# Kernel optimization log

Hardware: AMD Instinct MI355X
Metric: run time of the kernel (lower is better)

Reference implementation:

```python
import jax, jax.numpy as jnp
import numpy as np

ALPHA = 0.5
EPS = 1e-10

def setup_inputs() -> dict:
    key = jax.random.key(0)
    k1, k2, k3, k4 = jax.random.split(key, 4)
    B, S, H = 8, 2048, 768
    query_embs = jax.random.normal(k1, (B, S, H), dtype=jnp.float32)
    key_embs = jax.random.normal(k2, (B, S, H), dtype=jnp.float32)
    q_mask = (jax.random.uniform(k3, (B, S)) > 0.1).astype(jnp.float32)
    k_mask = (jax.random.uniform(k4, (B, S)) > 0.1).astype(jnp.float32)
    q_mask = q_mask.at[:, 0].set(1.0)
    k_mask = k_mask.at[:, 0].set(1.0)
    return {"query_embs": query_embs, "key_embs": key_embs,
            "q_mask": q_mask, "k_mask": k_mask, "gumbel_temp": 1.0}

def _l2norm(x):
    # torch F.normalize: x / max(||x||, eps-ish); use rsqrt with tiny floor
    n = jnp.sqrt(jnp.sum(x * x, axis=-1, keepdims=True))
    return x / jnp.maximum(n, 1e-12)

def reference(query_embs, key_embs, q_mask, k_mask, gumbel_temp):
    B, S, H = query_embs.shape
    q = _l2norm(query_embs)
    k = _l2norm(key_embs)
    sim = jnp.einsum('bqh,bkh->bqk', q, k)  # [B,S,S]
    # exponential distance decay w_{ij} = exp(-alpha*|i-j|)
    pos = jnp.arange(S)
    dist = jnp.abs(pos[:, None] - pos[None, :]).astype(sim.dtype)
    sim = sim * jnp.exp(-ALPHA * dist)
    valid = q_mask[:, :, None] * k_mask[:, None, :]  # [B,S,S]
    # eval path: no Gumbel noise
    noisy = sim / gumbel_temp
    noisy = noisy * valid - (1.0 - valid) * 1e9
    p = jax.nn.softmax(noisy, axis=-1)
    agg = jnp.einsum('bqk,bkh->bqh', p, k)
    scores = jnp.sum(q * agg, axis=-1) * q_mask  # [B,S]
    denom = jnp.maximum(jnp.sum(q_mask, axis=-1), 1.0)
    return jnp.sum(scores, axis=-1) / denom  # [B]
```

## Files before the change

kernel.cpp:

```cpp
#include <hip/hip_runtime.h>
#include <math.h>

#define SB 8
#define SS 2048
#define SH 768
#define ALPHA 0.5f

typedef __fp16 f16x8 __attribute__((ext_vector_type(8)));
typedef float f32x4 __attribute__((ext_vector_type(4)));

__device__ __forceinline__ float dot4(float4 a, float4 b) {
  return a.x*b.x + a.y*b.y + a.z*b.z + a.w*b.w;
}
__device__ __forceinline__ unsigned int pk2(float a, float b) {
  return __builtin_bit_cast(unsigned int, __builtin_amdgcn_cvt_pkrtz(a, b));
}

#define GLD(d, p, imm) \
  asm volatile("global_load_dwordx4 %0, %1, off offset:" #imm \
               : "=v"(d) : "v"(p) : "memory")
#define WAITV(n) asm volatile("s_waitcnt vmcnt(" #n ")" ::: "memory")
#define SB0() __builtin_amdgcn_sched_barrier(0)

#define ISSUE6(P, R0, R1, R2, R3, R4, R5) do { \
  GLD(R0, P, 0);   GLD(R1, P, 64);  GLD(R2, P, 128); \
  GLD(R3, P, 192); GLD(R4, P, 256); GLD(R5, P, 320); } while (0)

#define MFMA(a, b, c) __builtin_amdgcn_mfma_f32_16x16x32_f16(a, b, c, 0, 0, 0)

#define FTILE(t, R0, R1, R2, R3, R4, R5) do { \
  f32x4 da_ = {0,0,0,0}, db_ = {0,0,0,0}; \
  da_ = MFMA(a0, R0, da_); db_ = MFMA(a1, R1, db_); \
  da_ = MFMA(a2, R2, da_); db_ = MFMA(a3, R3, db_); \
  da_ = MFMA(a4, R4, da_); db_ = MFMA(a5, R5, db_); \
  sP[w][t][lane] = da_ + db_; } while (0)


__global__ __launch_bounds__(256) void kprep_kernel(
    const float* __restrict__ K, const float* __restrict__ km,
    const float* __restrict__ qm,
    __fp16* __restrict__ Khs, float* __restrict__ ksum,
    float* __restrict__ Nk, float* __restrict__ qsum) {
  __shared__ float4 red[4][3][64];
  int b = blockIdx.y, jc = blockIdx.x, t = threadIdx.x;
  int w = t >> 6, lane = t & 63;
  int j0 = jc * 32;
  float4 acc0 = {0,0,0,0}, acc1 = {0,0,0,0}, acc2 = {0,0,0,0};
  for (int jj = 0; jj < 8; ++jj) {
    int j = j0 + 8 * w + jj;
    const float4* rp = (const float4*)(K + ((size_t)b * SS + j) * SH);
    float4 a = rp[lane], b4 = rp[lane + 64], c4 = rp[lane + 128];
    float ssv = dot4(a, a) + dot4(b4, b4) + dot4(c4, c4);
    #pragma unroll
    for (int m = 1; m < 64; m <<= 1) ssv += __shfl_xor(ssv, m, 64);
    float kwj = km[b * SS + j] / fmaxf(sqrtf(ssv), 1e-12f);
    uint2* kr = (uint2*)(Khs + ((size_t)b * SS + j) * SH);
    kr[lane]       = make_uint2(pk2(a.x*kwj,  a.y*kwj),  pk2(a.z*kwj,  a.w*kwj));
    kr[lane + 64]  = make_uint2(pk2(b4.x*kwj, b4.y*kwj), pk2(b4.z*kwj, b4.w*kwj));
    kr[lane + 128] = make_uint2(pk2(c4.x*kwj, c4.y*kwj), pk2(c4.z*kwj, c4.w*kwj));
    acc0.x += a.x*kwj;  acc0.y += a.y*kwj;  acc0.z += a.z*kwj;  acc0.w += a.w*kwj;
    acc1.x += b4.x*kwj; acc1.y += b4.y*kwj; acc1.z += b4.z*kwj; acc1.w += b4.w*kwj;
    acc2.x += c4.x*kwj; acc2.y += c4.y*kwj; acc2.z += c4.z*kwj; acc2.w += c4.w*kwj;
  }
  red[w][0][lane] = acc0; red[w][1][lane] = acc1; red[w][2][lane] = acc2;
  __syncthreads();
  if (t < 192) {
    int s = t >> 6, l = t & 63;
    float4 r0 = red[0][s][l], r1 = red[1][s][l], r2 = red[2][s][l], r3 = red[3][s][l];
    float* kp = ksum + b * SH + (s * 64 + l) * 4;
    atomicAdd(kp + 0, r0.x+r1.x+r2.x+r3.x);
    atomicAdd(kp + 1, r0.y+r1.y+r2.y+r3.y);
    atomicAdd(kp + 2, r0.z+r1.z+r2.z+r3.z);
    atomicAdd(kp + 3, r0.w+r1.w+r2.w+r3.w);
  }
  if (t < 32) {
    float pkm = km[b * SS + j0 + t];
    float pqm = qm[b * SS + j0 + t];
    #pragma unroll
    for (int m = 1; m < 32; m <<= 1) {
      pkm += __shfl_xor(pkm, m, 64);
      pqm += __shfl_xor(pqm, m, 64);
    }
    if (t == 0) { atomicAdd(&Nk[b], pkm); atomicAdd(&qsum[b], pqm); }
  }
}

__global__ __launch_bounds__(256)
__attribute__((amdgpu_waves_per_eu(4, 4)))
void band_kernel(
    const float* __restrict__ Q, const __fp16* __restrict__ Khs,
    const float* __restrict__ temp, const float* __restrict__ qm,
    const float* __restrict__ ksum, const float* __restrict__ Nkp,
    const float* __restrict__ qsum,
    float* __restrict__ acc, int* __restrict__ cnt, float* __restrict__ out) {
  __shared__ f32x4 sP[4][5][64];
  __shared__ float sSS[4][16], sDD[4][16];
  __shared__ float tab_s[64];
  int tid = threadIdx.x;
  int w = tid >> 6, lane = tid & 63;
  int l15 = lane & 15, quad = lane >> 4;
  int blk = blockIdx.x;
  int work = (blk & 7) * 128 + (blk >> 3);
  int b = work >> 7;
  int i0 = (work & 127) * 16;

  if (tid < 64) {
    float invt = 1.0f / temp[0];
    tab_s[tid] = __expf(-ALPHA * fabsf((float)(tid - 31))) * invt;
  }
  float nk = Nkp[b];

  const char* qpB = (const char*)(Q + ((size_t)b * SS + i0 + l15) * SH
                                  + w * 192 + quad * 8);
  const float* ksb = ksum + (size_t)b * SH + w * 192 + quad * 8;
  float4 x0, x1, x2, x3, x4, x5, x6, x7, x8, x9, x10, x11;
  GLD(x0, qpB, 0);    GLD(x1, qpB, 16);   GLD(x2, qpB, 128);
  GLD(x3, qpB, 144);  GLD(x4, qpB, 256);  GLD(x5, qpB, 272);
  GLD(x6, qpB, 384);  GLD(x7, qpB, 400);  GLD(x8, qpB, 512);
  GLD(x9, qpB, 528);  GLD(x10, qpB, 640); GLD(x11, qpB, 656);
  float4 g0  = *(const float4*)(ksb + 0);
  float4 g1  = *(const float4*)(ksb + 4);
  float4 g2  = *(const float4*)(ksb + 32);
  float4 g3  = *(const float4*)(ksb + 36);
  float4 g4  = *(const float4*)(ksb + 64);
  float4 g5  = *(const float4*)(ksb + 68);
  float4 g6  = *(const float4*)(ksb + 96);
  float4 g7  = *(const float4*)(ksb + 100);
  float4 g8  = *(const float4*)(ksb + 128);
  float4 g9  = *(const float4*)(ksb + 132);
  float4 g10 = *(const float4*)(ksb + 160);
  float4 g11 = *(const float4*)(ksb + 164);
  WAITV(0); SB0();

  float ss = dot4(x0,x0) + dot4(x1,x1) + dot4(x2,x2) + dot4(x3,x3)
           + dot4(x4,x4) + dot4(x5,x5) + dot4(x6,x6) + dot4(x7,x7)
           + dot4(x8,x8) + dot4(x9,x9) + dot4(x10,x10) + dot4(x11,x11);
  float dd = dot4(x0,g0) + dot4(x1,g1) + dot4(x2,g2) + dot4(x3,g3)
           + dot4(x4,g4) + dot4(x5,g5) + dot4(x6,g6) + dot4(x7,g7)
           + dot4(x8,g8) + dot4(x9,g9) + dot4(x10,g10) + dot4(x11,g11);
  #define MKA(a, xA, xB) do { \
    uint4 u_ = make_uint4(pk2(xA.x, xA.y), pk2(xA.z, xA.w), \
                          pk2(xB.x, xB.y), pk2(xB.z, xB.w)); \
    a = __builtin_bit_cast(f16x8, u_); } while (0)
  f16x8 a0, a1, a2, a3, a4, a5;
  MKA(a0, x0, x1); MKA(a1, x2, x3); MKA(a2, x4, x5);
  MKA(a3, x6, x7); MKA(a4, x8, x9); MKA(a5, x10, x11);

  ss += __shfl_xor(ss, 16, 64); ss += __shfl_xor(ss, 32, 64);
  dd += __shfl_xor(dd, 16, 64); dd += __shfl_xor(dd, 32, 64);
  if (quad == 0) { sSS[w][l15] = ss; sDD[w][l15] = dd; }

  const __fp16* KbH = Khs + (size_t)b * SS * SH;
  int jc0 = min(max(i0 - 32 + l15, 0), SS - 1);
  int jc1 = min(max(i0 - 16 + l15, 0), SS - 1);
  int jc2 = i0 + l15;
  int jc3 = min(i0 + 16 + l15, SS - 1);
  int jc4 = min(i0 + 32 + l15, SS - 1);
  const char* pt0 = (const char*)(KbH + (size_t)jc0 * SH + w * 192 + quad * 8);
  const char* pt1 = (const char*)(KbH + (size_t)jc1 * SH + w * 192 + quad * 8);
  const char* pt2 = (const char*)(KbH + (size_t)jc2 * SH + w * 192 + quad * 8);
  const char* pt3 = (const char*)(KbH + (size_t)jc3 * SH + w * 192 + quad * 8);
  const char* pt4 = (const char*)(KbH + (size_t)jc4 * SH + w * 192 + quad * 8);

  f16x8 B0, B1, B2, B3, B4, B5, C0, C1, C2, C3, C4, C5;
  ISSUE6(pt0, B0, B1, B2, B3, B4, B5);
  ISSUE6(pt1, C0, C1, C2, C3, C4, C5);
  WAITV(6); SB0(); FTILE(0, B0, B1, B2, B3, B4, B5);
  ISSUE6(pt2, B0, B1, B2, B3, B4, B5);
  WAITV(6); SB0(); FTILE(1, C0, C1, C2, C3, C4, C5);
  ISSUE6(pt3, C0, C1, C2, C3, C4, C5);
  WAITV(6); SB0(); FTILE(2, B0, B1, B2, B3, B4, B5);
  ISSUE6(pt4, B0, B1, B2, B3, B4, B5);
  WAITV(6); SB0(); FTILE(3, C0, C1, C2, C3, C4, C5);
  WAITV(0); SB0(); FTILE(4, B0, B1, B2, B3, B4, B5);

  __syncthreads();

  float qws[4], d0s[4];
  #pragma unroll
  for (int reg = 0; reg < 4; ++reg) {
    int r = quad * 4 + reg;
    float ssr = sSS[0][r] + sSS[1][r] + sSS[2][r] + sSS[3][r];
    float ddr = sDD[0][r] + sDD[1][r] + sDD[2][r] + sDD[3][r];
    qws[reg] = qm[b * SS + i0 + r] / fmaxf(sqrtf(ssr), 1e-12f);
    d0s[reg] = ddr;
  }
  float an[4] = {0,0,0,0}, ad[4] = {0,0,0,0};
  #pragma unroll
  for (int t = 0; t < 5; ++t) {
    f32x4 v = sP[0][t][lane] + sP[1][t][lane] + sP[2][t][lane] + sP[3][t][lane];
    int j = i0 - 32 + 16 * t + l15;
    float vmask = ((unsigned)j < SS) ? 1.0f : 0.0f;
    int idxb = 16 * t + l15 - 1;
    #pragma unroll
    for (int reg = 0; reg < 4; ++reg) {
      float sv = v[reg] * qws[reg];
      int idx = min(max(idxb - quad * 4 - reg, 0), 63);
      float ev = (__expf(sv * tab_s[idx]) - 1.0f) * vmask;
      an[reg] += ev * sv;
      ad[reg] += ev;
    }
  }
  float tot = 0.f;
  #pragma unroll
  for (int reg = 0; reg < 4; ++reg) {
    float a = an[reg], e = ad[reg];
    a += __shfl_xor(a, 1, 64); a += __shfl_xor(a, 2, 64);
    a += __shfl_xor(a, 4, 64); a += __shfl_xor(a, 8, 64);
    e += __shfl_xor(e, 1, 64); e += __shfl_xor(e, 2, 64);
    e += __shfl_xor(e, 4, 64); e += __shfl_xor(e, 8, 64);
    tot += (qws[reg] * d0s[reg] + a) / (nk + e);
  }
  tot += __shfl_xor(tot, 16, 64);
  tot += __shfl_xor(tot, 32, 64);
  if (tid == 0) {
    atomicAdd(&acc[b], tot);
    __threadfence();
    if (atomicAdd(&cnt[b], 1) == 127) {
      float a2 = atomicAdd(&acc[b], 0.0f);
      out[b] = a2 / fmaxf(qsum[b], 1.0f);
    }
  }
}

extern "C" void kernel_launch(void* const* d_in, const int* in_sizes, int n_in,
                              void* d_out, int out_size, void* d_ws, size_t ws_size,
                              hipStream_t stream) {
  const float* Q    = (const float*)d_in[0];
  const float* K    = (const float*)d_in[1];
  const float* qm   = (const float*)d_in[2];
  const float* km   = (const float*)d_in[3];
  const float* temp = (const float*)d_in[4];
  float* outp = (float*)d_out;

  const size_t KHS_BYTES = (size_t)SB * SS * SH * 2;
  __fp16* Khs = (__fp16*)d_ws;
  float* ksum = (float*)((char*)d_ws + KHS_BYTES);
  float* Nk   = ksum + SB * SH;
  float* qsum = Nk + 8;
  float* accb = qsum + 8;
  int*   cnt  = (int*)(accb + 8);

  (void)hipMemsetAsync(ksum, 0, (SB * SH + 32) * sizeof(float), stream);

  kprep_kernel<<<dim3(64, SB), 256, 0, stream>>>(K, km, qm, Khs, ksum, Nk, qsum);
  band_kernel<<<1024, 256, 0, stream>>>(Q, Khs, temp, qm, ksum, Nk,
                                        qsum, accb, cnt, outp);
}
```

Before: 185.1 us.

## Split band kernel H dimension across eight waves instead of four

The band kernel now runs 512 threads per block, with each wave covering 96 of the hidden dimension instead of 192. The hand-scheduled inline-asm loads and waitcnt pipelining are replaced with plain compiler-scheduled loads. Partial MFMA tiles are combined through two shared-memory stages with an extra barrier. The aim is more waves in flight and fewer registers per wave, at the cost of losing the explicit load/compute overlap and adding shared-memory reduction traffic.

Result: no change. 181.9 us (-1.8%).

```diff
diff --git a/kernel.cpp b/kernel.cpp
--- a/kernel.cpp
+++ b/kernel.cpp
@@ -15,25 +15,7 @@
 __device__ __forceinline__ unsigned int pk2(float a, float b) {
   return __builtin_bit_cast(unsigned int, __builtin_amdgcn_cvt_pkrtz(a, b));
 }
-
-#define GLD(d, p, imm) \
-  asm volatile("global_load_dwordx4 %0, %1, off offset:" #imm \
-               : "=v"(d) : "v"(p) : "memory")
-#define WAITV(n) asm volatile("s_waitcnt vmcnt(" #n ")" ::: "memory")
-#define SB0() __builtin_amdgcn_sched_barrier(0)
-
-#define ISSUE6(P, R0, R1, R2, R3, R4, R5) do { \
-  GLD(R0, P, 0);   GLD(R1, P, 64);  GLD(R2, P, 128); \
-  GLD(R3, P, 192); GLD(R4, P, 256); GLD(R5, P, 320); } while (0)
-
 #define MFMA(a, b, c) __builtin_amdgcn_mfma_f32_16x16x32_f16(a, b, c, 0, 0, 0)
-
-#define FTILE(t, R0, R1, R2, R3, R4, R5) do { \
-  f32x4 da_ = {0,0,0,0}, db_ = {0,0,0,0}; \
-  da_ = MFMA(a0, R0, da_); db_ = MFMA(a1, R1, db_); \
-  da_ = MFMA(a2, R2, da_); db_ = MFMA(a3, R3, db_); \
-  da_ = MFMA(a4, R4, da_); db_ = MFMA(a5, R5, db_); \
-  sP[w][t][lane] = da_ + db_; } while (0)
 
 
 __global__ __launch_bounds__(256) void kprep_kernel(
@@ -85,16 +67,14 @@
   }
 }
 
-__global__ __launch_bounds__(256)
-__attribute__((amdgpu_waves_per_eu(4, 4)))
-void band_kernel(
+__global__ __launch_bounds__(512, 1) void band_kernel(
     const float* __restrict__ Q, const __fp16* __restrict__ Khs,
     const float* __restrict__ temp, const float* __restrict__ qm,
     const float* __restrict__ ksum, const float* __restrict__ Nkp,
     const float* __restrict__ qsum,
     float* __restrict__ acc, int* __restrict__ cnt, float* __restrict__ out) {
-  __shared__ f32x4 sP[4][5][64];
-  __shared__ float sSS[4][16], sDD[4][16];
+  __shared__ f32x4 sPc[4][5][64];
+  __shared__ float sSS[8][16], sDD[8][16];
   __shared__ float tab_s[64];
   int tid = threadIdx.x;
   int w = tid >> 6, lane = tid & 63;
@@ -109,86 +89,74 @@
     tab_s[tid] = __expf(-ALPHA * fabsf((float)(tid - 31))) * invt;
   }
   float nk = Nkp[b];
-
-  const char* qpB = (const char*)(Q + ((size_t)b * SS + i0 + l15) * SH
-                                  + w * 192 + quad * 8);
-  const float* ksb = ksum + (size_t)b * SH + w * 192 + quad * 8;
-  float4 x0, x1, x2, x3, x4, x5, x6, x7, x8, x9, x10, x11;
-  GLD(x0, qpB, 0);    GLD(x1, qpB, 16);   GLD(x2, qpB, 128);
-  GLD(x3, qpB, 144);  GLD(x4, qpB, 256);  GLD(x5, qpB, 272);
-  GLD(x6, qpB, 384);  GLD(x7, qpB, 400);  GLD(x8, qpB, 512);
-  GLD(x9, qpB, 528);  GLD(x10, qpB, 640); GLD(x11, qpB, 656);
-  float4 g0  = *(const float4*)(ksb + 0);
-  float4 g1  = *(const float4*)(ksb + 4);
-  float4 g2  = *(const float4*)(ksb + 32);
-  float4 g3  = *(const float4*)(ksb + 36);
-  float4 g4  = *(const float4*)(ksb + 64);
-  float4 g5  = *(const float4*)(ksb + 68);
-  float4 g6  = *(const float4*)(ksb + 96);
-  float4 g7  = *(const float4*)(ksb + 100);
-  float4 g8  = *(const float4*)(ksb + 128);
-  float4 g9  = *(const float4*)(ksb + 132);
-  float4 g10 = *(const float4*)(ksb + 160);
-  float4 g11 = *(const float4*)(ksb + 164);
-  WAITV(0); SB0();
-
-  float ss = dot4(x0,x0) + dot4(x1,x1) + dot4(x2,x2) + dot4(x3,x3)
-           + dot4(x4,x4) + dot4(x5,x5) + dot4(x6,x6) + dot4(x7,x7)
-           + dot4(x8,x8) + dot4(x9,x9) + dot4(x10,x10) + dot4(x11,x11);
-  float dd = dot4(x0,g0) + dot4(x1,g1) + dot4(x2,g2) + dot4(x3,g3)
-           + dot4(x4,g4) + dot4(x5,g5) + dot4(x6,g6) + dot4(x7,g7)
-           + dot4(x8,g8) + dot4(x9,g9) + dot4(x10,g10) + dot4(x11,g11);
+  float qm0 = qm[b * SS + i0 + quad * 4 + 0];
+  float qm1 = qm[b * SS + i0 + quad * 4 + 1];
+  float qm2 = qm[b * SS + i0 + quad * 4 + 2];
+  float qm3 = qm[b * SS + i0 + quad * 4 + 3];
+
+  const float* qp = Q + ((size_t)b * SS + i0 + l15) * SH + w * 96 + quad * 8;
+  const float* kp = ksum + (size_t)b * SH + w * 96 + quad * 8;
+  float4 x0 = *(const float4*)(qp + 0),  x1 = *(const float4*)(qp + 4);
+  float4 x2 = *(const float4*)(qp + 32), x3 = *(const float4*)(qp + 36);
+  float4 x4 = *(const float4*)(qp + 64), x5 = *(const float4*)(qp + 68);
+  float4 g0 = *(const float4*)(kp + 0),  g1 = *(const float4*)(kp + 4);
+  float4 g2 = *(const float4*)(kp + 32), g3 = *(const float4*)(kp + 36);
+  float4 g4 = *(const float4*)(kp + 64), g5 = *(const float4*)(kp + 68);
+  float ss = dot4(x0,x0) + dot4(x1,x1) + dot4(x2,x2)
+           + dot4(x3,x3) + dot4(x4,x4) + dot4(x5,x5);
+  float dd = dot4(x0,g0) + dot4(x1,g1) + dot4(x2,g2)
+           + dot4(x3,g3) + dot4(x4,g4) + dot4(x5,g5);
   #define MKA(a, xA, xB) do { \
     uint4 u_ = make_uint4(pk2(xA.x, xA.y), pk2(xA.z, xA.w), \
                           pk2(xB.x, xB.y), pk2(xB.z, xB.w)); \
     a = __builtin_bit_cast(f16x8, u_); } while (0)
-  f16x8 a0, a1, a2, a3, a4, a5;
+  f16x8 a0, a1, a2;
   MKA(a0, x0, x1); MKA(a1, x2, x3); MKA(a2, x4, x5);
-  MKA(a3, x6, x7); MKA(a4, x8, x9); MKA(a5, x10, x11);
-
   ss += __shfl_xor(ss, 16, 64); ss += __shfl_xor(ss, 32, 64);
   dd += __shfl_xor(dd, 16, 64); dd += __shfl_xor(dd, 32, 64);
   if (quad == 0) { sSS[w][l15] = ss; sDD[w][l15] = dd; }
 
   const __fp16* KbH = Khs + (size_t)b * SS * SH;
-  int jc0 = min(max(i0 - 32 + l15, 0), SS - 1);
-  int jc1 = min(max(i0 - 16 + l15, 0), SS - 1);
-  int jc2 = i0 + l15;
-  int jc3 = min(i0 + 16 + l15, SS - 1);
-  int jc4 = min(i0 + 32 + l15, SS - 1);
-  const char* pt0 = (const char*)(KbH + (size_t)jc0 * SH + w * 192 + quad * 8);
-  const char* pt1 = (const char*)(KbH + (size_t)jc1 * SH + w * 192 + quad * 8);
-  const char* pt2 = (const char*)(KbH + (size_t)jc2 * SH + w * 192 + quad * 8);
-  const char* pt3 = (const char*)(KbH + (size_t)jc3 * SH + w * 192 + quad * 8);
-  const char* pt4 = (const char*)(KbH + (size_t)jc4 * SH + w * 192 + quad * 8);
-
-  f16x8 B0, B1, B2, B3, B4, B5, C0, C1, C2, C3, C4, C5;
-  ISSUE6(pt0, B0, B1, B2, B3, B4, B5);
-  ISSUE6(pt1, C0, C1, C2, C3, C4, C5);
-  WAITV(6); SB0(); FTILE(0, B0, B1, B2, B3, B4, B5);
-  ISSUE6(pt2, B0, B1, B2, B3, B4, B5);
-  WAITV(6); SB0(); FTILE(1, C0, C1, C2, C3, C4, C5);
-  ISSUE6(pt3, C0, C1, C2, C3, C4, C5);
-  WAITV(6); SB0(); FTILE(2, B0, B1, B2, B3, B4, B5);
-  ISSUE6(pt4, B0, B1, B2, B3, B4, B5);
-  WAITV(6); SB0(); FTILE(3, C0, C1, C2, C3, C4, C5);
-  WAITV(0); SB0(); FTILE(4, B0, B1, B2, B3, B4, B5);
-
+  f32x4 d0t, d1t, d2t, d3t, d4t;
+  #define DOTILE(DT, T) do { \
+    int jc_ = min(max(i0 - 32 + 16 * (T) + l15, 0), SS - 1); \
+    const __fp16* bp_ = KbH + (size_t)jc_ * SH + w * 96 + quad * 8; \
+    f16x8 b0_ = *(const f16x8*)(bp_); \
+    f16x8 b1_ = *(const f16x8*)(bp_ + 32); \
+    f16x8 b2_ = *(const f16x8*)(bp_ + 64); \
+    f32x4 d_ = {0,0,0,0}; \
+    d_ = MFMA(a0, b0_, d_); d_ = MFMA(a1, b1_, d_); d_ = MFMA(a2, b2_, d_); \
+    DT = d_; } while (0)
+  DOTILE(d0t, 0); DOTILE(d1t, 1); DOTILE(d2t, 2); DOTILE(d3t, 3); DOTILE(d4t, 4);
+
+  if (w < 4) {
+    sPc[w][0][lane] = d0t; sPc[w][1][lane] = d1t; sPc[w][2][lane] = d2t;
+    sPc[w][3][lane] = d3t; sPc[w][4][lane] = d4t;
+  }
   __syncthreads();
+  if (w >= 4) {
+    sPc[w-4][0][lane] += d0t; sPc[w-4][1][lane] += d1t;
+    sPc[w-4][2][lane] += d2t; sPc[w-4][3][lane] += d3t;
+    sPc[w-4][4][lane] += d4t;
+  }
+  __syncthreads();
 
   float qws[4], d0s[4];
+  float qmr[4] = {qm0, qm1, qm2, qm3};
   #pragma unroll
   for (int reg = 0; reg < 4; ++reg) {
     int r = quad * 4 + reg;
-    float ssr = sSS[0][r] + sSS[1][r] + sSS[2][r] + sSS[3][r];
-    float ddr = sDD[0][r] + sDD[1][r] + sDD[2][r] + sDD[3][r];
-    qws[reg] = qm[b * SS + i0 + r] / fmaxf(sqrtf(ssr), 1e-12f);
+    float ssr = 0.f, ddr = 0.f;
+    #pragma unroll
+    for (int k = 0; k < 8; ++k) { ssr += sSS[k][r]; ddr += sDD[k][r]; }
+    qws[reg] = qmr[reg] / fmaxf(sqrtf(ssr), 1e-12f);
     d0s[reg] = ddr;
   }
   float an[4] = {0,0,0,0}, ad[4] = {0,0,0,0};
   #pragma unroll
   for (int t = 0; t < 5; ++t) {
-    f32x4 v = sP[0][t][lane] + sP[1][t][lane] + sP[2][t][lane] + sP[3][t][lane];
+    f32x4 v = sPc[0][t][lane] + sPc[1][t][lane]
+            + sPc[2][t][lane] + sPc[3][t][lane];
     int j = i0 - 32 + 16 * t + l15;
     float vmask = ((unsigned)j < SS) ? 1.0f : 0.0f;
     int idxb = 16 * t + l15 - 1;
@@ -244,6 +212,6 @@
   (void)hipMemsetAsync(ksum, 0, (SB * SH + 32) * sizeof(float), stream);
 
   kprep_kernel<<<dim3(64, SB), 256, 0, stream>>>(K, km, qm, Khs, ksum, Nk, qsum);
-  band_kernel<<<1024, 256, 0, stream>>>(Q, Khs, temp, qm, ksum, Nk,
+  band_kernel<<<1024, 512, 0, stream>>>(Q, Khs, temp, qm, ksum, Nk,
                                         qsum, accb, cnt, outp);
 }
```
